# Performance work log

Measured on AMD Instinct MI355X. Metric: run time of the kernel, lower is better.

## Reference

```python
import jax, jax.numpy as jnp
import numpy as np

# Module config (matches init_kwargs)
H, W = 512, 512          # in_dims
KH, KW = 32, 32          # kernel_dims
SH, SW = 16, 16          # stride
PH, PW = 8, 8            # padding
B = 64                   # batch
FULL_H, FULL_W = H + 2 * PH, W + 2 * PW            # 528, 528
NKH = 1 + (FULL_H - KH) // SH                      # 32
NKW = 1 + (FULL_W - KW) // SW                      # 32
NK = NKH * NKW                                     # 1024 output positions


def _patch_indices() -> np.ndarray:
    """Flat indices into the padded image for each sliding window.

    Reproduces the connectivity matrix columns of _create_connectivity_matrix:
    window k starts at (row*SH)*FULL_W + col*SW. Returns (NK, KH*KW) int32.
    """
    dr, dc = np.meshgrid(np.arange(KH), np.arange(KW), indexing="ij")
    off = (dr * FULL_W + dc).reshape(-1)                       # (KH*KW,)
    starts = (np.arange(NKH)[:, None] * SH * FULL_W
              + np.arange(NKW)[None, :] * SW).reshape(-1)      # (NK,)
    return (starts[:, None] + off[None, :]).astype(np.int32)


_IDX = jnp.asarray(_patch_indices())  # (NK, KH*KW), constant layout


def setup_inputs() -> dict:
    key = jax.random.key(0)
    kx, kw, kb = jax.random.split(key, 3)
    x = jax.random.normal(kx, (B, 1, H, W), dtype=jnp.float32)
    # Per-window weights = BSR values of the masked dense (padded_total, NK) matrix.
    # Xavier-normal scale of the underlying dense linear.
    std = float(np.sqrt(2.0 / (FULL_H * FULL_W + NK)))
    weight = jax.random.normal(kw, (NK, KH * KW), dtype=jnp.float32) * std
    bias = jax.random.normal(kb, (NK,), dtype=jnp.float32) * 0.01
    return {"x": x, "weight": weight, "bias": bias}


def reference(x, weight, bias):
    # x: (B, 1, H, W) -> pad -> flatten to (B, FULL_H*FULL_W)
    xp = jnp.pad(x, ((0, 0), (0, 0), (PH, PH), (PW, PW)))
    xf = xp.reshape(x.shape[0], FULL_H * FULL_W)
    # Gather the KHxKW window for every output position: (B, NK, KH*KW).
    patches = jnp.take(xf, _IDX, axis=1)
    # Untied locally-connected contraction (the block-sparse GEMM) + bias.
    out = jnp.einsum("bnk,nk->bn", patches, weight) + bias
    return out.reshape(x.shape[0], NKH, NKW)
```

## Files before the change

### kernel.cpp

```cpp
#include <hip/hip_runtime.h>

#define IMG_H 512
#define IMG_W 512
#define NKH 32
#define NKW 32
#define NK 1024
#define BATCH 64
#define NTT 33
#define NTILE (NTT * NTT)
#define NBLK (NTILE * 2)

__global__ __launch_bounds__(256, 4)
void bslc_main(const float* __restrict__ x,
               const float* __restrict__ w,
               float* __restrict__ P)
{
    __shared__ float4 xt[64][32];

    const int hw   = blockIdx.x;
    const int xcd  = hw & 7, slot = hw >> 3;
    const int q8   = NBLK >> 3, r8 = NBLK & 7;
    const int work = (xcd < r8 ? xcd * (q8 + 1)
                               : r8 * (q8 + 1) + (xcd - r8) * q8) + slot;

    const int bg  = work & 1;
    const int lin = work >> 1;
    const int tr  = lin / NTT, tc = lin % NTT;

    const int t = threadIdx.x, lane = t & 63, wv = t >> 6;

    const int r0 = tr * 16 - 8, c0 = tc * 16 - 8;
    const int kk = lane;
    const int rimg = r0 + (kk >> 2);
    const int cimg = c0 + (kk & 3) * 4;
    const bool interior = (tr >= 1) & (tr <= 31) & (tc >= 1) & (tc <= 31);
    const size_t xoff = (size_t)rimg * IMG_W + cimg;

    if (interior) {
#pragma unroll
        for (int i = 0; i < 8; ++i) {
            const int b = i * 4 + wv;
            const float4 v = *reinterpret_cast<const float4*>(
                x + (size_t)(bg * 32 + b) * (IMG_H * IMG_W) + xoff);
            xt[kk][(b + kk) & 31] = v;
        }
    } else {
        const bool ok = (rimg >= 0) & (rimg < IMG_H) & (cimg >= 0) & (cimg < IMG_W);
#pragma unroll
        for (int i = 0; i < 8; ++i) {
            const int b = i * 4 + wv;
            float4 v = make_float4(0.f, 0.f, 0.f, 0.f);
            if (ok)
                v = *reinterpret_cast<const float4*>(
                    x + (size_t)(bg * 32 + b) * (IMG_H * IMG_W) + xoff);
            xt[kk][(b + kk) & 31] = v;
        }
    }
    __syncthreads();

    const int qr = wv >> 1, qc = wv & 1;
    const int nr = tr - qr, nc = tc - qc;
    if (nr < 0 || nr >= NKH || nc < 0 || nc >= NKW) return;

    const int n    = nr * NKW + nc;
    const int half = lane >> 5;
    const int b    = lane & 31;
    const float* wb = w + (size_t)n * 1024
                    + (size_t)(qr * 16 + half * 8) * 32 + qc * 16;

    float a0 = 0.f, a1 = 0.f, a2 = 0.f, a3 = 0.f;
#pragma unroll
    for (int j = 0; j < 32; ++j) {
        const int kq = half * 32 + j;
        const float4 xv  = xt[kq][(b + kq) & 31];
        const float4 wv4 = *reinterpret_cast<const float4*>(
            wb + (j >> 2) * 32 + (j & 3) * 4);
        a0 = fmaf(xv.x, wv4.x, a0);
        a1 = fmaf(xv.y, wv4.y, a1);
        a2 = fmaf(xv.z, wv4.z, a2);
        a3 = fmaf(xv.w, wv4.w, a3);
    }
    float s = (a0 + a1) + (a2 + a3);
    s += __shfl_xor(s, 32, 64);
    if (half == 0)
        P[((size_t)(tr * NTT + tc) * 4 + wv) * 64 + bg * 32 + b] = s;
}

__global__ __launch_bounds__(256)
void bslc_reduce(const float* __restrict__ P,
                 const float* __restrict__ bias,
                 float* __restrict__ out)
{
    const int g = blockIdx.x * 256 + threadIdx.x;
    const int n = g >> 6;
    const int b = g & 63;
    const int nr = n >> 5, nc = n & 31;
    float s = bias[n];
#pragma unroll
    for (int qq = 0; qq < 4; ++qq) {
        const int tile = (nr + (qq >> 1)) * NTT + nc + (qq & 1);
        s += P[((size_t)tile * 4 + qq) * 64 + b];
    }
    out[(size_t)b * NK + n] = s;
}

extern "C" void kernel_launch(void* const* d_in, const int* in_sizes, int n_in,
                              void* d_out, int out_size, void* d_ws, size_t ws_size,
                              hipStream_t stream) {
    const float* x    = (const float*)d_in[0];
    const float* wgt  = (const float*)d_in[1];
    const float* bias = (const float*)d_in[2];
    float* out        = (float*)d_out;
    float* P          = (float*)d_ws;

    bslc_main<<<dim3(NBLK), 256, 0, stream>>>(x, wgt, P);
    bslc_reduce<<<dim3(BATCH * NK / 256), 256, 0, stream>>>(P, bias, out);
}
```

Baseline: 108.7 us.

## Use direct global-to-LDS loads, atomic accumulation, and smaller batch groups

Interior tiles now load the image through the global_load_lds builtin into an XOR-swizzled shared buffer. Each block handles 16 batch images instead of 32, which gives twice as many blocks and a higher occupancy hint. The separate partial-sum buffer and reduce kernel are replaced by an init kernel that writes the bias plus float atomicAdd from the main kernel. This removes the workspace round trip, but it adds atomic contention (four adds per output) and makes the summation order nondeterministic.

```diff
diff --git a/kernel.cpp b/kernel.cpp
--- a/kernel.cpp
+++ b/kernel.cpp
@@ -2,58 +2,73 @@
 
 #define IMG_H 512
 #define IMG_W 512
+#define IMG_SZ (IMG_H * IMG_W)
 #define NKH 32
 #define NKW 32
 #define NK 1024
 #define BATCH 64
 #define NTT 33
 #define NTILE (NTT * NTT)
-#define NBLK (NTILE * 2)
+#define BG 4
+#define NBLK (NTILE * BG)
 
-__global__ __launch_bounds__(256, 4)
+typedef __attribute__((address_space(3))) char lds_char_t;
+typedef const __attribute__((address_space(1))) char g_char_t;
+
+__global__ __launch_bounds__(256)
+void bslc_init(const float* __restrict__ bias, float* __restrict__ out)
+{
+    const int g = blockIdx.x * 256 + threadIdx.x;
+    out[g] = bias[g & (NK - 1)];
+}
+
+__global__ __launch_bounds__(256, 8)
 void bslc_main(const float* __restrict__ x,
                const float* __restrict__ w,
-               float* __restrict__ P)
+               float* __restrict__ out)
 {
-    __shared__ float4 xt[64][32];
+    __shared__ float4 xs[16 * 64];
 
-    const int hw   = blockIdx.x;
-    const int xcd  = hw & 7, slot = hw >> 3;
-    const int q8   = NBLK >> 3, r8 = NBLK & 7;
+    const int hw = blockIdx.x;
+    const int xcd = hw & 7, sl = hw >> 3;
+    const int q8 = NBLK >> 3, r8 = NBLK & 7;
     const int work = (xcd < r8 ? xcd * (q8 + 1)
-                               : r8 * (q8 + 1) + (xcd - r8) * q8) + slot;
+                               : r8 * (q8 + 1) + (xcd - r8) * q8) + sl;
 
-    const int bg  = work & 1;
-    const int lin = work >> 1;
-    const int tr  = lin / NTT, tc = lin % NTT;
+    const int bg  = work & 3;
+    const int lin = work >> 2;
+    const int tr = lin / NTT, tc = lin % NTT;
 
     const int t = threadIdx.x, lane = t & 63, wv = t >> 6;
 
     const int r0 = tr * 16 - 8, c0 = tc * 16 - 8;
-    const int kk = lane;
-    const int rimg = r0 + (kk >> 2);
-    const int cimg = c0 + (kk & 3) * 4;
     const bool interior = (tr >= 1) & (tr <= 31) & (tc >= 1) & (tc <= 31);
-    const size_t xoff = (size_t)rimg * IMG_W + cimg;
 
     if (interior) {
 #pragma unroll
-        for (int i = 0; i < 8; ++i) {
-            const int b = i * 4 + wv;
-            const float4 v = *reinterpret_cast<const float4*>(
-                x + (size_t)(bg * 32 + b) * (IMG_H * IMG_W) + xoff);
-            xt[kk][(b + kk) & 31] = v;
+        for (int ii = 0; ii < 4; ++ii) {
+            const int bl = 4 * ii + wv;
+            const int c  = lane ^ bl;
+            const int rimg = r0 + (c >> 2);
+            const int cimg = c0 + (c & 3) * 4;
+            const float* gp = x + (size_t)(bg * 16 + bl) * IMG_SZ
+                            + (size_t)rimg * IMG_W + cimg;
+            __builtin_amdgcn_global_load_lds(
+                (g_char_t*)gp, (lds_char_t*)&xs[bl * 64], 16, 0, 0);
         }
     } else {
-        const bool ok = (rimg >= 0) & (rimg < IMG_H) & (cimg >= 0) & (cimg < IMG_W);
 #pragma unroll
-        for (int i = 0; i < 8; ++i) {
-            const int b = i * 4 + wv;
+        for (int ii = 0; ii < 4; ++ii) {
+            const int bl = 4 * ii + wv;
+            const int c  = lane ^ bl;
+            const int rimg = r0 + (c >> 2);
+            const int cimg = c0 + (c & 3) * 4;
             float4 v = make_float4(0.f, 0.f, 0.f, 0.f);
-            if (ok)
+            if (rimg >= 0 && rimg < IMG_H && cimg >= 0 && cimg < IMG_W)
                 v = *reinterpret_cast<const float4*>(
-                    x + (size_t)(bg * 32 + b) * (IMG_H * IMG_W) + xoff);
-            xt[kk][(b + kk) & 31] = v;
+                    x + (size_t)(bg * 16 + bl) * IMG_SZ
+                      + (size_t)rimg * IMG_W + cimg);
+            xs[bl * 64 + lane] = v;
         }
     }
     __syncthreads();
@@ -61,47 +76,29 @@
     const int qr = wv >> 1, qc = wv & 1;
     const int nr = tr - qr, nc = tc - qc;
     if (nr < 0 || nr >= NKH || nc < 0 || nc >= NKW) return;
+    const int n = nr * NKW + nc;
 
-    const int n    = nr * NKW + nc;
-    const int half = lane >> 5;
-    const int b    = lane & 31;
-    const float* wb = w + (size_t)n * 1024
-                    + (size_t)(qr * 16 + half * 8) * 32 + qc * 16;
+    const int p  = lane >> 4;
+    const int bl = lane & 15;
+    const float* wq = w + (size_t)n * 1024 + (size_t)(qr * 16) * 32 + qc * 16;
 
     float a0 = 0.f, a1 = 0.f, a2 = 0.f, a3 = 0.f;
 #pragma unroll
-    for (int j = 0; j < 32; ++j) {
-        const int kq = half * 32 + j;
-        const float4 xv  = xt[kq][(b + kq) & 31];
+    for (int j = 0; j < 16; ++j) {
+        const int kq = p * 16 + j;
+        const float4 xv  = xs[bl * 64 + (kq ^ bl)];
         const float4 wv4 = *reinterpret_cast<const float4*>(
-            wb + (j >> 2) * 32 + (j & 3) * 4);
+            wq + (kq >> 2) * 32 + (kq & 3) * 4);
         a0 = fmaf(xv.x, wv4.x, a0);
         a1 = fmaf(xv.y, wv4.y, a1);
         a2 = fmaf(xv.z, wv4.z, a2);
         a3 = fmaf(xv.w, wv4.w, a3);
     }
     float s = (a0 + a1) + (a2 + a3);
+    s += __shfl_xor(s, 16, 64);
     s += __shfl_xor(s, 32, 64);
-    if (half == 0)
-        P[((size_t)(tr * NTT + tc) * 4 + wv) * 64 + bg * 32 + b] = s;
-}
-
-__global__ __launch_bounds__(256)
-void bslc_reduce(const float* __restrict__ P,
-                 const float* __restrict__ bias,
-                 float* __restrict__ out)
-{
-    const int g = blockIdx.x * 256 + threadIdx.x;
-    const int n = g >> 6;
-    const int b = g & 63;
-    const int nr = n >> 5, nc = n & 31;
-    float s = bias[n];
-#pragma unroll
-    for (int qq = 0; qq < 4; ++qq) {
-        const int tile = (nr + (qq >> 1)) * NTT + nc + (qq & 1);
-        s += P[((size_t)tile * 4 + qq) * 64 + b];
-    }
-    out[(size_t)b * NK + n] = s;
+    if (p == 0)
+        atomicAdd(&out[(size_t)(bg * 16 + bl) * NK + n], s);
 }
 
 extern "C" void kernel_launch(void* const* d_in, const int* in_sizes, int n_in,
@@ -111,8 +108,7 @@
     const float* wgt  = (const float*)d_in[1];
     const float* bias = (const float*)d_in[2];
     float* out        = (float*)d_out;
-    float* P          = (float*)d_ws;
 
-    bslc_main<<<dim3(NBLK), 256, 0, stream>>>(x, wgt, P);
-    bslc_reduce<<<dim3(BATCH * NK / 256), 256, 0, stream>>>(P, bias, out);
+    bslc_init<<<dim3(BATCH * NK / 256), 256, 0, stream>>>(bias, out);
+    bslc_main<<<dim3(NBLK), 256, 0, stream>>>(x, wgt, out);
 }
```

After: 112.5 us. 1.03x slower.
